# Optimization experiments

Measured on AMD Instinct MI355X. Metric: run time of the kernel, lower is better.

The kernel has to match this reference:

```python
import jax, jax.numpy as jnp
import numpy as np

N_NODES = 50000
N_EDGES = 800000
IN_DIM = 128
HID_DIM = 128
N_CLASSES = 40


def setup_inputs() -> dict:
    key = jax.random.key(0)
    ks = jax.random.split(key, 12)
    s = 0.05
    inp = {
        "X": jax.random.normal(ks[0], (N_NODES, IN_DIM), jnp.float32),
        "A": jax.random.randint(ks[1], (2, N_EDGES), 0, N_NODES, dtype=jnp.int64),
        "W0": jax.random.normal(ks[2], (HID_DIM, IN_DIM), jnp.float32) * s,
        "b0": jnp.zeros((HID_DIM,), jnp.float32),
        "W1": jax.random.normal(ks[3], (HID_DIM, HID_DIM), jnp.float32) * s,
        "b1": jnp.zeros((HID_DIM,), jnp.float32),
        "W2": jax.random.normal(ks[4], (HID_DIM, HID_DIM), jnp.float32) * s,
        "b2": jnp.zeros((HID_DIM,), jnp.float32),
        "W3": jax.random.normal(ks[5], (HID_DIM, HID_DIM), jnp.float32) * s,
        "b3": jnp.zeros((HID_DIM,), jnp.float32),
        "Wf": jax.random.normal(ks[6], (N_CLASSES, HID_DIM), jnp.float32) * s,
        "bf": jnp.zeros((N_CLASSES,), jnp.float32),
    }
    return inp


def _gcn_conv(x, W, b, src, dst):
    # FrobeniusNormGCNConv: normalize weight by Frobenius norm, then standard GCNConv
    Wn = W / jnp.linalg.norm(W)
    h = x @ Wn.T  # [N, out]
    # gcn_norm with self-loops (edge weight 1.0): deg over targets + 1 self loop
    ones = jnp.ones((dst.shape[0],), h.dtype)
    deg = jax.ops.segment_sum(ones, dst, num_segments=N_NODES) + 1.0
    dinv = jax.lax.rsqrt(deg)  # [N]
    norm = dinv[src] * dinv[dst]  # [E]
    # scatter-add of normalized source messages into targets
    agg = jax.ops.segment_sum(norm[:, None] * h[src], dst, num_segments=N_NODES)
    # self-loop contribution: dinv[i]^2 * h[i]; bias added after aggregation
    return agg + (dinv * dinv)[:, None] * h + b


def reference(X, A, W0, b0, W1, b1, W2, b2, W3, b3, Wf, bf):
    src, dst = A[0], A[1]
    h = _gcn_conv(X, W0, b0, src, dst)
    skip = h
    for W, b in ((W1, b1), (W2, b2), (W3, b3)):
        h = _gcn_conv(h, W, b, src, dst)
        h = jax.nn.relu(h)
        h = h + skip  # residual skip (dropout identity in eval mode)
        skip = h
    return h @ Wf.T + bf
```

## Files before the change

### kernel.cpp

```cpp
#include <hip/hip_runtime.h>

#define N_NODES_C 50000
#define N_EDGES_C 800000
#define DIM 128
#define NCLS 40
#define NBUK 32
#define BCAP 32768
#define NOCT 8

typedef __attribute__((ext_vector_type(8))) short bf16x8;
typedef __attribute__((ext_vector_type(4))) float f32x4;

__device__ inline float bf2f(unsigned short u) {
    union { unsigned int i; float f; } c;
    c.i = ((unsigned int)u) << 16;
    return c.f;
}
__device__ inline unsigned short f2bf(float f) {
    union { float f; unsigned int i; } c;
    c.f = f;
    unsigned int x = c.i;
    x += 0x7fffu + ((x >> 16) & 1u);
    return (unsigned short)(x >> 16);
}
__device__ inline void unp8(const uint4& g, float* f) {
    f[0] = __uint_as_float(g.x << 16); f[1] = __uint_as_float(g.x & 0xFFFF0000u);
    f[2] = __uint_as_float(g.y << 16); f[3] = __uint_as_float(g.y & 0xFFFF0000u);
    f[4] = __uint_as_float(g.z << 16); f[5] = __uint_as_float(g.z & 0xFFFF0000u);
    f[6] = __uint_as_float(g.w << 16); f[7] = __uint_as_float(g.w & 0xFFFF0000u);
}

__global__ __launch_bounds__(256) void k_pre(const float* __restrict__ W0,
                                             const float* __restrict__ W1,
                                             const float* __restrict__ W2,
                                             const float* __restrict__ W3,
                                             unsigned short* __restrict__ Wb,
                                             float* __restrict__ scale_inv,
                                             int* __restrict__ gcount) {
    int b = blockIdx.x;
    if (b < 64) {
        int m = b >> 4;
        int idx = (b & 15) * 256 + threadIdx.x;
        const float* W = m == 0 ? W0 : m == 1 ? W1 : m == 2 ? W2 : W3;
        float4 v = reinterpret_cast<const float4*>(W)[idx];
        reinterpret_cast<ushort4*>(Wb + (size_t)m * DIM * DIM)[idx] =
            make_ushort4(f2bf(v.x), f2bf(v.y), f2bf(v.z), f2bf(v.w));
        return;
    }
    b -= 64;
    if (b == 0 && threadIdx.x < NBUK) gcount[threadIdx.x] = 0;
    const float* W = b == 0 ? W0 : b == 1 ? W1 : b == 2 ? W2 : W3;
    float s = 0.f;
    for (int i = threadIdx.x; i < DIM * DIM; i += 256) {
        float v = W[i];
        s += v * v;
    }
    #pragma unroll
    for (int off = 32; off >= 1; off >>= 1) s += __shfl_down(s, off);
    __shared__ float red[4];
    int lane = threadIdx.x & 63, wid = threadIdx.x >> 6;
    if (lane == 0) red[wid] = s;
    __syncthreads();
    if (threadIdx.x == 0) {
        float tot = red[0] + red[1] + red[2] + red[3];
        scale_inv[b] = 1.0f / sqrtf(tot);
    }
}

__global__ __launch_bounds__(256) void k_bucket(const int* __restrict__ A,
                                                int* __restrict__ gcount,
                                                unsigned int* __restrict__ ebuk, int E) {
    __shared__ int cnt[NBUK];
    __shared__ int gbase[NBUK];
    int tid = threadIdx.x;
    if (tid < NBUK) cnt[tid] = 0;
    __syncthreads();
    int e0 = blockIdx.x * 1024;
    int s[4], d[4], b[4], r[4];
    #pragma unroll
    for (int j = 0; j < 4; ++j) {
        int e = e0 + j * 256 + tid;
        if (e < E) {
            s[j] = A[e];
            d[j] = A[E + e];
            b[j] = (int)(((unsigned long long)(unsigned)d[j] * NBUK) / N_NODES_C);
            r[j] = atomicAdd(&cnt[b[j]], 1);
        } else {
            b[j] = -1;
        }
    }
    __syncthreads();
    if (tid < NBUK) gbase[tid] = atomicAdd(&gcount[tid], cnt[tid]);
    __syncthreads();
    #pragma unroll
    for (int j = 0; j < 4; ++j) {
        if (b[j] >= 0) {
            int pos = gbase[b[j]] + r[j];
            if (pos < BCAP)
                ebuk[(size_t)b[j] * BCAP + pos] =
                    ((unsigned)d[j] << 16) | (unsigned)s[j];
        }
    }
}

__global__ __launch_bounds__(512) void k_csr(const unsigned int* __restrict__ ebuk,
                                             const int* __restrict__ gcount,
                                             int* __restrict__ ptr,
                                             float* __restrict__ dinv,
                                             unsigned short* __restrict__ esrc) {
    __shared__ int dlo[NOCT][1568];
    __shared__ int gc[NBUK];
    __shared__ int wsum2[8], wpre2[8];
    int k = blockIdx.x;
    int tid = threadIdx.x;
    int base = (k * N_NODES_C + NBUK - 1) / NBUK;
    int next = ((k + 1) * N_NODES_C + NBUK - 1) / NBUK;
    int sz = next - base;

    for (int i = tid; i < NOCT * 1568; i += 512) (&dlo[0][0])[i] = 0;
    if (tid < NBUK) gc[tid] = min(gcount[tid], BCAP);
    __syncthreads();

    int count = gc[k];
    int bucket_base = 0;
    #pragma unroll
    for (int j = 0; j < NBUK; ++j) bucket_base += (j < k) ? gc[j] : 0;
    const unsigned int* eb = ebuk + (size_t)k * BCAP;

    for (int i = tid; i < count; i += 512) {
        unsigned v = eb[i];
        int d = (int)(v >> 16) - base;
        int src = (int)(v & 0xFFFFu);
        int oct = (src * NOCT) / N_NODES_C;
        atomicAdd(&dlo[oct][d], 1);
    }
    __syncthreads();

    int degloc[4];
    int mysum = 0;
    #pragma unroll
    for (int c = 0; c < 4; ++c) {
        int i = tid * 4 + c;
        int ds = 0;
        if (i < sz) {
            #pragma unroll
            for (int o = 0; o < NOCT; ++o) ds += dlo[o][i];
        }
        degloc[c] = ds;
        mysum += ds;
    }
    int lane = tid & 63, wid = tid >> 6;
    int sc = mysum;
    #pragma unroll
    for (int off = 1; off < 64; off <<= 1) {
        int t = __shfl_up(sc, off);
        if (lane >= off) sc += t;
    }
    if (lane == 63) wsum2[wid] = sc;
    __syncthreads();
    if (tid == 0) {
        int a = 0;
        #pragma unroll
        for (int w = 0; w < 8; ++w) { wpre2[w] = a; a += wsum2[w]; }
    }
    __syncthreads();
    int run = wpre2[wid] + sc - mysum;
    #pragma unroll
    for (int c = 0; c < 4; ++c) {
        int i = tid * 4 + c;
        if (i < sz) {
            ptr[base + i] = bucket_base + run;
            dinv[base + i] = rsqrtf((float)degloc[c] + 1.0f);
            int r = run;
            #pragma unroll
            for (int o = 0; o < NOCT; ++o) {
                int t = dlo[o][i];
                dlo[o][i] = r;
                r += t;
            }
            run += degloc[c];
        }
    }
    if (k == NBUK - 1 && tid == 511) ptr[N_NODES_C] = bucket_base + run;
    __syncthreads();

    for (int i = tid; i < count; i += 512) {
        unsigned v = eb[i];
        int d = (int)(v >> 16) - base;
        int src = (int)(v & 0xFFFFu);
        int oct = (src * NOCT) / N_NODES_C;
        int pos = atomicAdd(&dlo[oct][d], 1);
        esrc[bucket_base + pos] = (unsigned short)src;
    }
}

template <bool F32A>
__global__ __launch_bounds__(256) void k_gemm_mfma(const void* __restrict__ Xp,
                                                   const unsigned short* __restrict__ Wb,
                                                   const float* __restrict__ scale_ptr,
                                                   const float* __restrict__ dinv,
                                                   unsigned short* __restrict__ Gb, int N) {
    int tid = threadIdx.x;
    int w = tid >> 6;
    int l = tid & 63;
    int l15 = l & 15;
    int lg = l >> 4;
    int arow = blockIdx.x * 64 + w * 16 + l15;
    if (arow >= N) arow = N - 1;
    float scale = scale_ptr[0];

    f32x4 acc[8];
    #pragma unroll
    for (int ct = 0; ct < 8; ++ct) acc[ct] = f32x4{0.f, 0.f, 0.f, 0.f};

    #pragma unroll
    for (int kc = 0; kc < 4; ++kc) {
        int ko = kc * 32 + lg * 8;
        bf16x8 a;
        if (F32A) {
            const float4* xf = reinterpret_cast<const float4*>(
                (const float*)Xp + (size_t)arow * DIM + ko);
            float4 u = xf[0], v = xf[1];
            a[0] = (short)f2bf(u.x); a[1] = (short)f2bf(u.y);
            a[2] = (short)f2bf(u.z); a[3] = (short)f2bf(u.w);
            a[4] = (short)f2bf(v.x); a[5] = (short)f2bf(v.y);
            a[6] = (short)f2bf(v.z); a[7] = (short)f2bf(v.w);
        } else {
            a = *reinterpret_cast<const bf16x8*>(
                (const unsigned short*)Xp + (size_t)arow * DIM + ko);
        }
        #pragma unroll
        for (int ct = 0; ct < 8; ++ct) {
            bf16x8 b = *reinterpret_cast<const bf16x8*>(&Wb[(size_t)(ct * 16 + l15) * DIM + ko]);
            acc[ct] = __builtin_amdgcn_mfma_f32_16x16x32_bf16(a, b, acc[ct], 0, 0, 0);
        }
    }
    int outrow0 = blockIdx.x * 64 + w * 16 + lg * 4;
    #pragma unroll
    for (int r = 0; r < 4; ++r) {
        int row = outrow0 + r;
        if (row < N) {
            float dv = dinv[row] * scale;
            #pragma unroll
            for (int ct = 0; ct < 8; ++ct)
                Gb[(size_t)row * DIM + ct * 16 + l15] = f2bf(acc[ct][r] * dv);
        }
    }
}

template <bool RELU>
__global__ __launch_bounds__(256) void k_agg(const unsigned short* __restrict__ Gb,
                                             const float* __restrict__ bias,
                                             const float* __restrict__ dinv,
                                             const int* __restrict__ ptr,
                                             const unsigned short* __restrict__ esrc,
                                             const unsigned short* __restrict__ skipb,
                                             unsigned short* __restrict__ outb) {
    int n = blockIdx.x * 4 + (threadIdx.x >> 6);
    int l = threadIdx.x & 63;
    int grp = l >> 4, li = l & 15;
    const uint4* __restrict__ Gv = reinterpret_cast<const uint4*>(Gb);
    int beg = ptr[n], end = ptr[n + 1];
    float acc[8] = {};
    float t[8];
    int e = beg;
    for (; e + 16 <= end; e += 16) {
        int s0 = esrc[e + grp];
        int s1 = esrc[e + 4 + grp];
        int s2 = esrc[e + 8 + grp];
        int s3 = esrc[e + 12 + grp];
        uint4 g0 = Gv[(size_t)s0 * 16 + li];
        uint4 g1 = Gv[(size_t)s1 * 16 + li];
        uint4 g2 = Gv[(size_t)s2 * 16 + li];
        uint4 g3 = Gv[(size_t)s3 * 16 + li];
        unp8(g0, t);
        #pragma unroll
        for (int j = 0; j < 8; ++j) acc[j] += t[j];
        unp8(g1, t);
        #pragma unroll
        for (int j = 0; j < 8; ++j) acc[j] += t[j];
        unp8(g2, t);
        #pragma unroll
        for (int j = 0; j < 8; ++j) acc[j] += t[j];
        unp8(g3, t);
        #pragma unroll
        for (int j = 0; j < 8; ++j) acc[j] += t[j];
    }
    for (; e + 4 <= end; e += 4) {
        int s0 = esrc[e + grp];
        uint4 g0 = Gv[(size_t)s0 * 16 + li];
        unp8(g0, t);
        #pragma unroll
        for (int j = 0; j < 8; ++j) acc[j] += t[j];
    }
    int rem = end - e;
    if (grp < rem) {
        int s0 = esrc[e + grp];
        uint4 g0 = Gv[(size_t)s0 * 16 + li];
        unp8(g0, t);
        #pragma unroll
        for (int j = 0; j < 8; ++j) acc[j] += t[j];
    }
    #pragma unroll
    for (int j = 0; j < 8; ++j) {
        acc[j] += __shfl_xor(acc[j], 16);
        acc[j] += __shfl_xor(acc[j], 32);
    }
    if (grp == 0) {
        float di = dinv[n];
        uint4 gu = Gv[(size_t)n * 16 + li];
        float gs[8];
        unp8(gu, gs);
        const float4* b4 = reinterpret_cast<const float4*>(bias);
        float4 ba = b4[li * 2], bb = b4[li * 2 + 1];
        float bv[8] = {ba.x, ba.y, ba.z, ba.w, bb.x, bb.y, bb.z, bb.w};
        float v[8];
        #pragma unroll
        for (int j = 0; j < 8; ++j) v[j] = fmaf(di, acc[j] + gs[j], bv[j]);
        if (RELU) {
            uint4 su = reinterpret_cast<const uint4*>(skipb)[(size_t)n * 16 + li];
            float ss[8];
            unp8(su, ss);
            #pragma unroll
            for (int j = 0; j < 8; ++j) v[j] = fmaxf(v[j], 0.f) + ss[j];
        }
        uint4 o;
        o.x = (unsigned)f2bf(v[0]) | ((unsigned)f2bf(v[1]) << 16);
        o.y = (unsigned)f2bf(v[2]) | ((unsigned)f2bf(v[3]) << 16);
        o.z = (unsigned)f2bf(v[4]) | ((unsigned)f2bf(v[5]) << 16);
        o.w = (unsigned)f2bf(v[6]) | ((unsigned)f2bf(v[7]) << 16);
        reinterpret_cast<uint4*>(outb)[(size_t)n * 16 + li] = o;
    }
}

__global__ __launch_bounds__(256) void k_final(const unsigned short* __restrict__ Hb,
                                               const float* __restrict__ Wf,
                                               const float* __restrict__ bf,
                                               float* __restrict__ out, int N) {
    __shared__ float Xs[16][68];
    __shared__ float Ws[16][64];
    int tid = threadIdx.x;
    int n0 = blockIdx.x * 64;
    int tx = tid & 15;
    int ty = tid >> 4;
    float acc[4][4] = {};
    for (int k0 = 0; k0 < DIM; k0 += 16) {
        {
            int j = tid >> 2, kq = tid & 3;
            int row = n0 + j;
            if (row >= N) row = N - 1;
            ushort4 x4 = *reinterpret_cast<const ushort4*>(&Hb[(size_t)row * DIM + k0 + kq * 4]);
            Xs[kq * 4 + 0][j] = bf2f(x4.x);
            Xs[kq * 4 + 1][j] = bf2f(x4.y);
            Xs[kq * 4 + 2][j] = bf2f(x4.z);
            Xs[kq * 4 + 3][j] = bf2f(x4.w);
        }
        {
            int o = tid >> 2, kq = tid & 3;
            int om = o < NCLS ? o : o - NCLS;
            const float4 w4 = *reinterpret_cast<const float4*>(&Wf[(size_t)om * DIM + k0 + kq * 4]);
            Ws[kq * 4 + 0][o] = w4.x;
            Ws[kq * 4 + 1][o] = w4.y;
            Ws[kq * 4 + 2][o] = w4.z;
            Ws[kq * 4 + 3][o] = w4.w;
        }
        __syncthreads();
        #pragma unroll
        for (int k = 0; k < 16; ++k) {
            float4 w = *reinterpret_cast<const float4*>(&Ws[k][tx * 4]);
            float4 x = *reinterpret_cast<const float4*>(&Xs[k][ty * 4]);
            float xv[4] = {x.x, x.y, x.z, x.w};
            #pragma unroll
            for (int i = 0; i < 4; ++i) {
                acc[i][0] = fmaf(xv[i], w.x, acc[i][0]);
                acc[i][1] = fmaf(xv[i], w.y, acc[i][1]);
                acc[i][2] = fmaf(xv[i], w.z, acc[i][2]);
                acc[i][3] = fmaf(xv[i], w.w, acc[i][3]);
            }
        }
        __syncthreads();
    }
    if (tx >= 10) return;
    float4 b4 = make_float4(bf[tx * 4], bf[tx * 4 + 1], bf[tx * 4 + 2], bf[tx * 4 + 3]);
    #pragma unroll
    for (int i = 0; i < 4; ++i) {
        int row = n0 + ty * 4 + i;
        if (row < N) {
            float* op = &out[(size_t)row * NCLS + tx * 4];
            op[0] = acc[i][0] + b4.x;
            op[1] = acc[i][1] + b4.y;
            op[2] = acc[i][2] + b4.z;
            op[3] = acc[i][3] + b4.w;
        }
    }
}

extern "C" void kernel_launch(void* const* d_in, const int* in_sizes, int n_in,
                              void* d_out, int out_size, void* d_ws, size_t ws_size,
                              hipStream_t stream) {
    (void)in_sizes; (void)n_in; (void)out_size; (void)ws_size;
    const float* X  = (const float*)d_in[0];
    const int*   A  = (const int*)d_in[1];
    const float* W0 = (const float*)d_in[2];
    const float* b0 = (const float*)d_in[3];
    const float* W1 = (const float*)d_in[4];
    const float* b1 = (const float*)d_in[5];
    const float* W2 = (const float*)d_in[6];
    const float* b2 = (const float*)d_in[7];
    const float* W3 = (const float*)d_in[8];
    const float* b3 = (const float*)d_in[9];
    const float* Wf = (const float*)d_in[10];
    const float* bf = (const float*)d_in[11];
    float* out = (float*)d_out;

    char* base_ws = (char*)d_ws;
    size_t off = 0;
    auto alloc = [&](size_t bytes) -> char* {
        char* p = base_ws + off;
        off = (off + bytes + 255) & ~(size_t)255;
        return p;
    };
    float* scale_inv = (float*)alloc(4 * sizeof(float));
    int*   ptr    = (int*)alloc((N_NODES_C + 1) * sizeof(int));
    float* dinv   = (float*)alloc(N_NODES_C * sizeof(float));
    int*   gcount = (int*)alloc(NBUK * sizeof(int));
    unsigned int*   ebuk = (unsigned int*)alloc((size_t)NBUK * BCAP * sizeof(unsigned int));
    unsigned short* esrc = (unsigned short*)alloc((size_t)N_EDGES_C * sizeof(unsigned short));
    unsigned short* Gb  = (unsigned short*)alloc((size_t)N_NODES_C * DIM * sizeof(unsigned short));
    unsigned short* Hb1 = (unsigned short*)alloc((size_t)N_NODES_C * DIM * sizeof(unsigned short));
    unsigned short* Hb2 = (unsigned short*)alloc((size_t)N_NODES_C * DIM * sizeof(unsigned short));
    unsigned short* Wb  = (unsigned short*)alloc((size_t)4 * DIM * DIM * sizeof(unsigned short));

    k_pre<<<68, 256, 0, stream>>>(W0, W1, W2, W3, Wb, scale_inv, gcount);
    k_bucket<<<(N_EDGES_C + 1023) / 1024, 256, 0, stream>>>(A, gcount, ebuk, N_EDGES_C);
    k_csr<<<NBUK, 512, 0, stream>>>(ebuk, gcount, ptr, dinv, esrc);

    const int gemm_grid = (N_NODES_C + 63) / 64;
    const int agg_grid  = N_NODES_C / 4;

    k_gemm_mfma<true><<<gemm_grid, 256, 0, stream>>>(X, Wb + 0 * DIM * DIM, scale_inv + 0, dinv, Gb, N_NODES_C);
    k_agg<false><<<agg_grid, 256, 0, stream>>>(Gb, b0, dinv, ptr, esrc, nullptr, Hb1);
    k_gemm_mfma<false><<<gemm_grid, 256, 0, stream>>>(Hb1, Wb + 1 * DIM * DIM, scale_inv + 1, dinv, Gb, N_NODES_C);
    k_agg<true><<<agg_grid, 256, 0, stream>>>(Gb, b1, dinv, ptr, esrc, Hb1, Hb2);
    k_gemm_mfma<false><<<gemm_grid, 256, 0, stream>>>(Hb2, Wb + 2 * DIM * DIM, scale_inv + 2, dinv, Gb, N_NODES_C);
    k_agg<true><<<agg_grid, 256, 0, stream>>>(Gb, b2, dinv, ptr, esrc, Hb2, Hb1);
    k_gemm_mfma<false><<<gemm_grid, 256, 0, stream>>>(Hb1, Wb + 3 * DIM * DIM, scale_inv + 3, dinv, Gb, N_NODES_C);
    k_agg<true><<<agg_grid, 256, 0, stream>>>(Gb, b3, dinv, ptr, esrc, Hb1, Hb2);
    k_final<<<(N_NODES_C + 63) / 64, 256, 0, stream>>>(Hb2, Wf, bf, out, N_NODES_C);
}
```

Baseline: 311.1 us.

## Use MFMA for final projection, XCD-remap aggregation blocks, pack CSR counters

The final classifier GEMM is rewritten to use bf16 MFMA, with Wf converted to bf16 in the pre-kernel. Aggregation blocks are remapped so each XCD processes a contiguous node range, and the self, skip and bias loads are hoisted before the edge loop to overlap latency. The CSR build doubles the number of source partitions by packing two 16-bit counters per shared word, which improves locality of source ordering within each destination. These trade some precision in the final layer for less FMA and shared-memory work.

```diff
diff --git a/kernel.cpp b/kernel.cpp
--- a/kernel.cpp
+++ b/kernel.cpp
@@ -6,7 +6,7 @@
 #define NCLS 40
 #define NBUK 32
 #define BCAP 32768
-#define NOCT 8
+#define NOCT 16
 
 typedef __attribute__((ext_vector_type(8))) short bf16x8;
 typedef __attribute__((ext_vector_type(4))) float f32x4;
@@ -34,7 +34,9 @@
                                              const float* __restrict__ W1,
                                              const float* __restrict__ W2,
                                              const float* __restrict__ W3,
+                                             const float* __restrict__ Wf,
                                              unsigned short* __restrict__ Wb,
+                                             unsigned short* __restrict__ Wfb,
                                              float* __restrict__ scale_inv,
                                              int* __restrict__ gcount) {
     int b = blockIdx.x;
@@ -48,6 +50,14 @@
         return;
     }
     b -= 64;
+    if (b < 5) {
+        int idx = b * 256 + threadIdx.x;
+        float4 v = reinterpret_cast<const float4*>(Wf)[idx];
+        reinterpret_cast<ushort4*>(Wfb)[idx] =
+            make_ushort4(f2bf(v.x), f2bf(v.y), f2bf(v.z), f2bf(v.w));
+        return;
+    }
+    b -= 5;
     if (b == 0 && threadIdx.x < NBUK) gcount[threadIdx.x] = 0;
     const float* W = b == 0 ? W0 : b == 1 ? W1 : b == 2 ? W2 : W3;
     float s = 0.f;
@@ -108,7 +118,7 @@
                                              int* __restrict__ ptr,
                                              float* __restrict__ dinv,
                                              unsigned short* __restrict__ esrc) {
-    __shared__ int dlo[NOCT][1568];
+    __shared__ unsigned int dlo[NOCT / 2][1568];
     __shared__ int gc[NBUK];
     __shared__ int wsum2[8], wpre2[8];
     int k = blockIdx.x;
@@ -117,7 +127,7 @@
     int next = ((k + 1) * N_NODES_C + NBUK - 1) / NBUK;
     int sz = next - base;
 
-    for (int i = tid; i < NOCT * 1568; i += 512) (&dlo[0][0])[i] = 0;
+    for (int i = tid; i < (NOCT / 2) * 1568; i += 512) (&dlo[0][0])[i] = 0;
     if (tid < NBUK) gc[tid] = min(gcount[tid], BCAP);
     __syncthreads();
 
@@ -132,7 +142,7 @@
         int d = (int)(v >> 16) - base;
         int src = (int)(v & 0xFFFFu);
         int oct = (src * NOCT) / N_NODES_C;
-        atomicAdd(&dlo[oct][d], 1);
+        atomicAdd(&dlo[oct >> 1][d], 1u << ((oct & 1) * 16));
     }
     __syncthreads();
 
@@ -144,7 +154,10 @@
         int ds = 0;
         if (i < sz) {
             #pragma unroll
-            for (int o = 0; o < NOCT; ++o) ds += dlo[o][i];
+            for (int p = 0; p < NOCT / 2; ++p) {
+                unsigned v = dlo[p][i];
+                ds += (int)(v & 0xFFFFu) + (int)(v >> 16);
+            }
         }
         degloc[c] = ds;
         mysum += ds;
@@ -173,10 +186,11 @@
             dinv[base + i] = rsqrtf((float)degloc[c] + 1.0f);
             int r = run;
             #pragma unroll
-            for (int o = 0; o < NOCT; ++o) {
-                int t = dlo[o][i];
-                dlo[o][i] = r;
-                r += t;
+            for (int p = 0; p < NOCT / 2; ++p) {
+                unsigned v = dlo[p][i];
+                int lo = (int)(v & 0xFFFFu), hi = (int)(v >> 16);
+                dlo[p][i] = (unsigned)r | ((unsigned)(r + lo) << 16);
+                r += lo + hi;
             }
             run += degloc[c];
         }
@@ -189,7 +203,8 @@
         int d = (int)(v >> 16) - base;
         int src = (int)(v & 0xFFFFu);
         int oct = (src * NOCT) / N_NODES_C;
-        int pos = atomicAdd(&dlo[oct][d], 1);
+        unsigned old = atomicAdd(&dlo[oct >> 1][d], 1u << ((oct & 1) * 16));
+        int pos = (int)((old >> ((oct & 1) * 16)) & 0xFFFFu);
         esrc[bucket_base + pos] = (unsigned short)src;
     }
 }
@@ -256,11 +271,24 @@
                                              const unsigned short* __restrict__ esrc,
                                              const unsigned short* __restrict__ skipb,
                                              unsigned short* __restrict__ outb) {
-    int n = blockIdx.x * 4 + (threadIdx.x >> 6);
+    int orig = blockIdx.x;
+    int xcd = orig & 7;
+    int idx = orig >> 3;
+    int wgid = (xcd < 4 ? xcd * 1563 : 4 * 1563 + (xcd - 4) * 1562) + idx;
+
+    int n = wgid * 4 + (threadIdx.x >> 6);
     int l = threadIdx.x & 63;
     int grp = l >> 4, li = l & 15;
     const uint4* __restrict__ Gv = reinterpret_cast<const uint4*>(Gb);
     int beg = ptr[n], end = ptr[n + 1];
+
+    uint4 gu = Gv[(size_t)n * 16 + li];
+    uint4 su;
+    if (RELU) su = reinterpret_cast<const uint4*>(skipb)[(size_t)n * 16 + li];
+    const float4* b4p = reinterpret_cast<const float4*>(bias);
+    float4 ba = b4p[li * 2], bb = b4p[li * 2 + 1];
+    float di = dinv[n];
+
     float acc[8] = {};
     float t[8];
     int e = beg;
@@ -307,18 +335,13 @@
         acc[j] += __shfl_xor(acc[j], 32);
     }
     if (grp == 0) {
-        float di = dinv[n];
-        uint4 gu = Gv[(size_t)n * 16 + li];
         float gs[8];
         unp8(gu, gs);
-        const float4* b4 = reinterpret_cast<const float4*>(bias);
-        float4 ba = b4[li * 2], bb = b4[li * 2 + 1];
         float bv[8] = {ba.x, ba.y, ba.z, ba.w, bb.x, bb.y, bb.z, bb.w};
         float v[8];
         #pragma unroll
         for (int j = 0; j < 8; ++j) v[j] = fmaf(di, acc[j] + gs[j], bv[j]);
         if (RELU) {
-            uint4 su = reinterpret_cast<const uint4*>(skipb)[(size_t)n * 16 + li];
             float ss[8];
             unp8(su, ss);
             #pragma unroll
@@ -334,63 +357,44 @@
 }
 
 __global__ __launch_bounds__(256) void k_final(const unsigned short* __restrict__ Hb,
-                                               const float* __restrict__ Wf,
+                                               const unsigned short* __restrict__ Wfb,
                                                const float* __restrict__ bf,
                                                float* __restrict__ out, int N) {
-    __shared__ float Xs[16][68];
-    __shared__ float Ws[16][64];
     int tid = threadIdx.x;
-    int n0 = blockIdx.x * 64;
-    int tx = tid & 15;
-    int ty = tid >> 4;
-    float acc[4][4] = {};
-    for (int k0 = 0; k0 < DIM; k0 += 16) {
-        {
-            int j = tid >> 2, kq = tid & 3;
-            int row = n0 + j;
-            if (row >= N) row = N - 1;
-            ushort4 x4 = *reinterpret_cast<const ushort4*>(&Hb[(size_t)row * DIM + k0 + kq * 4]);
-            Xs[kq * 4 + 0][j] = bf2f(x4.x);
-            Xs[kq * 4 + 1][j] = bf2f(x4.y);
-            Xs[kq * 4 + 2][j] = bf2f(x4.z);
-            Xs[kq * 4 + 3][j] = bf2f(x4.w);
-        }
-        {
-            int o = tid >> 2, kq = tid & 3;
-            int om = o < NCLS ? o : o - NCLS;
-            const float4 w4 = *reinterpret_cast<const float4*>(&Wf[(size_t)om * DIM + k0 + kq * 4]);
-            Ws[kq * 4 + 0][o] = w4.x;
-            Ws[kq * 4 + 1][o] = w4.y;
-            Ws[kq * 4 + 2][o] = w4.z;
-            Ws[kq * 4 + 3][o] = w4.w;
-        }
-        __syncthreads();
-        #pragma unroll
-        for (int k = 0; k < 16; ++k) {
-            float4 w = *reinterpret_cast<const float4*>(&Ws[k][tx * 4]);
-            float4 x = *reinterpret_cast<const float4*>(&Xs[k][ty * 4]);
-            float xv[4] = {x.x, x.y, x.z, x.w};
+    int w = tid >> 6;
+    int l = tid & 63;
+    int l15 = l & 15;
+    int lg = l >> 4;
+    int arow = blockIdx.x * 64 + w * 16 + l15;
+    if (arow >= N) arow = N - 1;
+
+    f32x4 acc[3];
+    #pragma unroll
+    for (int ct = 0; ct < 3; ++ct) acc[ct] = f32x4{0.f, 0.f, 0.f, 0.f};
+
+    #pragma unroll
+    for (int kc = 0; kc < 4; ++kc) {
+        int ko = kc * 32 + lg * 8;
+        bf16x8 a = *reinterpret_cast<const bf16x8*>(&Hb[(size_t)arow * DIM + ko]);
+        #pragma unroll
+        for (int ct = 0; ct < 3; ++ct) {
+            int wr = ct * 16 + l15;
+            if (wr >= NCLS) wr = 0;
+            bf16x8 b = *reinterpret_cast<const bf16x8*>(&Wfb[(size_t)wr * DIM + ko]);
+            acc[ct] = __builtin_amdgcn_mfma_f32_16x16x32_bf16(a, b, acc[ct], 0, 0, 0);
+        }
+    }
+    int outrow0 = blockIdx.x * 64 + w * 16 + lg * 4;
+    #pragma unroll
+    for (int ct = 0; ct < 3; ++ct) {
+        int c = ct * 16 + l15;
+        if (c < NCLS) {
+            float bias = bf[c];
             #pragma unroll
-            for (int i = 0; i < 4; ++i) {
-                acc[i][0] = fmaf(xv[i], w.x, acc[i][0]);
-                acc[i][1] = fmaf(xv[i], w.y, acc[i][1]);
-                acc[i][2] = fmaf(xv[i], w.z, acc[i][2]);
-                acc[i][3] = fmaf(xv[i], w.w, acc[i][3]);
+            for (int r = 0; r < 4; ++r) {
+                int row = outrow0 + r;
+                if (row < N) out[(size_t)row * NCLS + c] = acc[ct][r] + bias;
             }
-        }
-        __syncthreads();
-    }
-    if (tx >= 10) return;
-    float4 b4 = make_float4(bf[tx * 4], bf[tx * 4 + 1], bf[tx * 4 + 2], bf[tx * 4 + 3]);
-    #pragma unroll
-    for (int i = 0; i < 4; ++i) {
-        int row = n0 + ty * 4 + i;
-        if (row < N) {
-            float* op = &out[(size_t)row * NCLS + tx * 4];
-            op[0] = acc[i][0] + b4.x;
-            op[1] = acc[i][1] + b4.y;
-            op[2] = acc[i][2] + b4.z;
-            op[3] = acc[i][3] + b4.w;
         }
     }
 }
@@ -430,8 +434,9 @@
     unsigned short* Hb1 = (unsigned short*)alloc((size_t)N_NODES_C * DIM * sizeof(unsigned short));
     unsigned short* Hb2 = (unsigned short*)alloc((size_t)N_NODES_C * DIM * sizeof(unsigned short));
     unsigned short* Wb  = (unsigned short*)alloc((size_t)4 * DIM * DIM * sizeof(unsigned short));
-
-    k_pre<<<68, 256, 0, stream>>>(W0, W1, W2, W3, Wb, scale_inv, gcount);
+    unsigned short* Wfb = (unsigned short*)alloc((size_t)NCLS * DIM * sizeof(unsigned short));
+
+    k_pre<<<73, 256, 0, stream>>>(W0, W1, W2, W3, Wf, Wb, Wfb, scale_inv, gcount);
     k_bucket<<<(N_EDGES_C + 1023) / 1024, 256, 0, stream>>>(A, gcount, ebuk, N_EDGES_C);
     k_csr<<<NBUK, 512, 0, stream>>>(ebuk, gcount, ptr, dinv, esrc);
 
@@ -446,5 +451,5 @@
     k_agg<true><<<agg_grid, 256, 0, stream>>>(Gb, b2, dinv, ptr, esrc, Hb2, Hb1);
     k_gemm_mfma<false><<<gemm_grid, 256, 0, stream>>>(Hb1, Wb + 3 * DIM * DIM, scale_inv + 3, dinv, Gb, N_NODES_C);
     k_agg<true><<<agg_grid, 256, 0, stream>>>(Gb, b3, dinv, ptr, esrc, Hb1, Hb2);
-    k_final<<<(N_NODES_C + 63) / 64, 256, 0, stream>>>(Hb2, Wf, bf, out, N_NODES_C);
-}
+    k_final<<<(N_NODES_C + 63) / 64, 256, 0, stream>>>(Hb2, Wfb, bf, out, N_NODES_C);
+}
```

After: 299.1 us. 3.9% less time.
